# Kernel tuning notes

Hardware: AMD Instinct MI355X
Metric: run time of the kernel (lower is better)

Reference implementation:

```python
import jax, jax.numpy as jnp
import numpy as np

N_NODES = 50000


def _sage_conv(x, src, dst, W_l, b_l, W_r, n_nodes):
    # mean-aggregate neighbor (source) features onto targets
    msg = x[src]                                   # [E, d_in] gather
    agg = jax.ops.segment_sum(msg, dst, num_segments=n_nodes)   # [N, d_in]
    deg = jax.ops.segment_sum(jnp.ones((src.shape[0],), x.dtype), dst,
                              num_segments=n_nodes)
    agg = agg / jnp.clip(deg, 1.0, None)[:, None]  # mean with deg>=1 clamp (PyG)
    # out = lin_l(agg) + lin_r(x)   (bias lives in lin_l)
    return agg @ W_l.T + b_l + x @ W_r.T


def setup_inputs() -> dict:
    key = jax.random.key(0)
    ks = jax.random.split(key, 8)
    d_in, d_hid, d_out = 128, 256, 128
    n_edges = 800000
    x = jax.random.normal(ks[0], (N_NODES, d_in), dtype=jnp.float32)
    edge_index = jax.random.randint(ks[1], (2, n_edges), 0, N_NODES, dtype=jnp.int32)
    def glorot(k, shape):
        lim = float(np.sqrt(6.0 / (shape[0] + shape[1])))
        return jax.random.uniform(k, shape, jnp.float32, -lim, lim)
    return {
        "x": x,
        "edge_index": edge_index,
        "W1l": glorot(ks[2], (d_hid, d_in)),
        "b1": jnp.zeros((d_hid,), jnp.float32),
        "W1r": glorot(ks[3], (d_hid, d_in)),
        "W2l": glorot(ks[4], (d_out, d_hid)),
        "b2": jnp.zeros((d_out,), jnp.float32),
        "W2r": glorot(ks[5], (d_out, d_hid)),
    }


def reference(x, edge_index, W1l, b1, W1r, W2l, b2, W2r):
    src, dst = edge_index[0], edge_index[1]
    h = jax.nn.relu(_sage_conv(x, src, dst, W1l, b1, W1r, N_NODES))
    out = _sage_conv(h, src, dst, W2l, b2, W2r, N_NODES)
    return out
```

## Files before the change

kernel.cpp:

```cpp
#include <hip/hip_runtime.h>
#include <hip/hip_bf16.h>

#define NN 50000
#define NN_PAD 50176
#define NE 800000
#define NB 196
#define CAP 6144
#define EPB 4096

typedef __attribute__((ext_vector_type(8))) short short8;
typedef __attribute__((ext_vector_type(4))) float f32x4;
typedef __attribute__((ext_vector_type(2))) float f32x2;

__device__ __forceinline__ unsigned short f2bf(float f) {
    union { float f; unsigned u; } v; v.f = f;
    unsigned u = v.u;
    return (unsigned short)((u + 0x7fffu + ((u >> 16) & 1u)) >> 16);
}
__device__ __forceinline__ float bfu_lo(unsigned u) {
    union { unsigned u; float f; } v; v.u = u << 16; return v.f;
}
__device__ __forceinline__ float bfu_hi(unsigned u) {
    union { unsigned u; float f; } v; v.u = u & 0xffff0000u; return v.f;
}


__global__ void k_setup_part(const float* __restrict__ W1l, const float* __restrict__ W1r,
                             const float* __restrict__ W2l, const float* __restrict__ W2r,
                             unsigned short* __restrict__ W1pk, unsigned short* __restrict__ W2pk,
                             const float4* __restrict__ x4, unsigned short* __restrict__ Apk,
                             unsigned char* __restrict__ x_f8,
                             const int* __restrict__ src, const int* __restrict__ dst,
                             int* __restrict__ gcursor, unsigned* __restrict__ pairs) {
    int blk = blockIdx.x, t = threadIdx.x;
    if (blk < NB) {
        __shared__ int cnt[256];
        __shared__ int cur[256];
        __shared__ int base[256];
        cnt[t] = 0; cur[t] = 0;
        __syncthreads();
        int e0 = blk * EPB;
        int eend = min(e0 + EPB, NE);
        for (int e = e0 + t; e < eend; e += 256)
            atomicAdd(&cnt[dst[e] >> 8], 1);
        __syncthreads();
        if (t < NB && cnt[t] > 0) base[t] = t * CAP + atomicAdd(&gcursor[t], cnt[t]);
        __syncthreads();
        for (int e = e0 + t; e < eend; e += 256) {
            int s = src[e], d = dst[e];
            int bk = d >> 8;
            int pos = base[bk] + atomicAdd(&cur[bk], 1);
            if (pos < (bk + 1) * CAP) pairs[pos] = ((unsigned)s << 8) | (unsigned)(d & 255);
        }
    } else if (blk < 260) {
        int tid = (blk - 196) * 256 + t;
        int table = tid >> 13;
        int r = tid & 8191;
        int lane = r & 63, ni = (r >> 6) & 3, ks = (r >> 8) & 7, g = r >> 11;
        int lm = lane & 15, lq = lane >> 4;
        int o = g * 64 + ni * 16 + lm;
        int k = ks * 32 + lq * 8;
        unsigned short v[8];
        if (table == 0) {
            if (k < 128) {
#pragma unroll
                for (int j = 0; j < 8; ++j) v[j] = f2bf(W1l[o * 128 + k + j]);
            } else {
#pragma unroll
                for (int j = 0; j < 8; ++j) v[j] = f2bf(W1r[o * 128 + k - 128 + j]);
            }
            *(uint4*)(W1pk + (size_t)r * 8) = *(const uint4*)v;
        } else {
            if (o < 128) {
#pragma unroll
                for (int j = 0; j < 8; ++j) v[j] = f2bf(W2l[o * 256 + k + j]);
            } else {
#pragma unroll
                for (int j = 0; j < 8; ++j) v[j] = f2bf(W2r[(o - 128) * 256 + k + j]);
            }
            *(uint4*)(W2pk + (size_t)r * 8) = *(const uint4*)v;
        }
    } else {
        int gid = (blk - 260) * 256 + t;
        int n = gid >> 5, c = gid & 31;
        float4 v = x4[(size_t)n * 32 + c];
        unsigned short o[4];
        o[0] = f2bf(v.x); o[1] = f2bf(v.y); o[2] = f2bf(v.z); o[3] = f2bf(v.w);
        int k = 128 + c * 4;
        int ks = k >> 5, lq = (k >> 3) & 3, j0 = k & 7;
        int tile = n >> 6, r = n & 63, mi = r >> 4, lm = r & 15;
        *(uint2*)(Apk + (size_t)tile * 16384 +
                  ((size_t)((ks * 4 + mi) * 64 + lm + 16 * lq)) * 8 + j0) = *(const uint2*)o;
        unsigned p = (unsigned)__builtin_amdgcn_cvt_pk_fp8_f32(v.x, v.y, 0, false);
        p = (unsigned)__builtin_amdgcn_cvt_pk_fp8_f32(v.z, v.w, (int)p, true);
        *(unsigned*)(x_f8 + (size_t)n * 128 + c * 4) = p;
    }
}

__global__ void k_build(const int* __restrict__ gcursor, const unsigned* __restrict__ pairs,
                        unsigned* __restrict__ meta, unsigned short* __restrict__ esrc) {
    __shared__ int buf[256];
    __shared__ int ldeg[256];
    __shared__ int cur[256];
    __shared__ int sh_base, sh_cnt;
    __shared__ unsigned short lsrc[CAP];
    int b = blockIdx.x, t = threadIdx.x;
    int c = (t < NB) ? min(gcursor[t], CAP) : 0;
    buf[t] = c;
    __syncthreads();
#pragma unroll
    for (int o = 1; o < 256; o <<= 1) {
        int add = (t >= o) ? buf[t - o] : 0;
        __syncthreads();
        buf[t] += add;
        __syncthreads();
    }
    if (t == b) { sh_cnt = c; sh_base = buf[b] - c; }
    ldeg[t] = 0;
    __syncthreads();
    int cnt = sh_cnt, base = sh_base;
    for (int e = t; e < cnt; e += 256)
        atomicAdd(&ldeg[pairs[(size_t)b * CAP + e] & 255u], 1);
    __syncthreads();
    int v = ldeg[t];
    buf[t] = v;
    __syncthreads();
#pragma unroll
    for (int o = 1; o < 256; o <<= 1) {
        int add = (t >= o) ? buf[t - o] : 0;
        __syncthreads();
        buf[t] += add;
        __syncthreads();
    }
    int lst = buf[t] - v;
    cur[t] = lst;
    int node = b * 256 + t;
    meta[node] = (node < NN) ? ((unsigned)(base + lst) | ((unsigned)v << 20)) : 0u;
    __syncthreads();
    for (int e = t; e < cnt; e += 256) {
        unsigned p = pairs[(size_t)b * CAP + e];
        int pos = atomicAdd(&cur[p & 255u], 1);
        lsrc[pos] = (unsigned short)(p >> 8);
    }
    __syncthreads();
    for (int e = t; e < cnt; e += 256) esrc[base + e] = lsrc[e];
}

__global__ void k_agg1(const uint2* __restrict__ xf8, const unsigned* __restrict__ meta,
                       const unsigned short* __restrict__ esrc,
                       unsigned short* __restrict__ Apk) {
    int gid = blockIdx.x * blockDim.x + threadIdx.x;
    int n = gid >> 4, c = gid & 15;
    unsigned mt = meta[n];
    int st = (int)(mt & 0xFFFFFu), dg = (int)(mt >> 20);
    float acc[8] = {0.f, 0.f, 0.f, 0.f, 0.f, 0.f, 0.f, 0.f};
    int i = 0;
    for (; i + 2 <= dg; i += 2) {
        int s0 = esrc[st + i], s1 = esrc[st + i + 1];
        uint2 q0 = xf8[(size_t)s0 * 16 + c];
        uint2 q1 = xf8[(size_t)s1 * 16 + c];
        f32x2 a0 = __builtin_amdgcn_cvt_pk_f32_fp8(q0.x, false);
        f32x2 a1 = __builtin_amdgcn_cvt_pk_f32_fp8(q0.x, true);
        f32x2 a2 = __builtin_amdgcn_cvt_pk_f32_fp8(q0.y, false);
        f32x2 a3 = __builtin_amdgcn_cvt_pk_f32_fp8(q0.y, true);
        f32x2 b0 = __builtin_amdgcn_cvt_pk_f32_fp8(q1.x, false);
        f32x2 b1 = __builtin_amdgcn_cvt_pk_f32_fp8(q1.x, true);
        f32x2 b2 = __builtin_amdgcn_cvt_pk_f32_fp8(q1.y, false);
        f32x2 b3 = __builtin_amdgcn_cvt_pk_f32_fp8(q1.y, true);
        acc[0] += a0.x + b0.x; acc[1] += a0.y + b0.y;
        acc[2] += a1.x + b1.x; acc[3] += a1.y + b1.y;
        acc[4] += a2.x + b2.x; acc[5] += a2.y + b2.y;
        acc[6] += a3.x + b3.x; acc[7] += a3.y + b3.y;
    }
    if (i < dg) {
        int s = esrc[st + i];
        uint2 q0 = xf8[(size_t)s * 16 + c];
        f32x2 a0 = __builtin_amdgcn_cvt_pk_f32_fp8(q0.x, false);
        f32x2 a1 = __builtin_amdgcn_cvt_pk_f32_fp8(q0.x, true);
        f32x2 a2 = __builtin_amdgcn_cvt_pk_f32_fp8(q0.y, false);
        f32x2 a3 = __builtin_amdgcn_cvt_pk_f32_fp8(q0.y, true);
        acc[0] += a0.x; acc[1] += a0.y;
        acc[2] += a1.x; acc[3] += a1.y;
        acc[4] += a2.x; acc[5] += a2.y;
        acc[6] += a3.x; acc[7] += a3.y;
    }
    float invd = 1.0f / (float)max(dg, 1);
    unsigned short o[8];
#pragma unroll
    for (int j = 0; j < 8; ++j) o[j] = f2bf(acc[j] * invd);
    int ks = c >> 2, lq = c & 3;
    int tile = n >> 6, r = n & 63, mi = r >> 4, lm = r & 15;
    *(uint4*)(Apk + (size_t)tile * 16384 +
              ((size_t)((ks * 4 + mi) * 64 + lm + 16 * lq)) * 8) = *(const uint4*)o;
}

__global__ __launch_bounds__(256, 2) void k_gemm12(
        const unsigned short* __restrict__ Apk,
        const unsigned short* __restrict__ W1pk, const unsigned short* __restrict__ W2pk,
        const float* __restrict__ b1, const float* __restrict__ b2,
        unsigned char* __restrict__ y2f8, unsigned short* __restrict__ Sbf) {
    __shared__ unsigned short T[16384];
    int t = threadIdx.x, blk = blockIdx.x;
    int wave = t >> 6, lane = t & 63;
    int lm = lane & 15, lq = lane >> 4;
    int pbase = lm * 4 + lq;

    short8 w[8][4];
    {
        const unsigned short* wb = W1pk + (size_t)wave * 16384;
#pragma unroll
        for (int ks = 0; ks < 8; ++ks)
#pragma unroll
            for (int ni = 0; ni < 4; ++ni)
                w[ks][ni] = *(const short8*)(wb + ((size_t)((ks * 4 + ni) * 64 + lane)) * 8);
    }

    const unsigned short* apk = Apk + (size_t)blk * 16384;
    f32x4 acc1[4][4];
#pragma unroll
    for (int mi = 0; mi < 4; ++mi)
#pragma unroll
        for (int ni = 0; ni < 4; ++ni) acc1[mi][ni] = (f32x4){0.f, 0.f, 0.f, 0.f};
#pragma unroll
    for (int ks = 0; ks < 8; ++ks) {
        short8 a[4];
#pragma unroll
        for (int mi = 0; mi < 4; ++mi)
            a[mi] = *(const short8*)(apk + ((size_t)((ks * 4 + mi) * 64 + lane)) * 8);
#pragma unroll
        for (int mi = 0; mi < 4; ++mi)
#pragma unroll
            for (int ni = 0; ni < 4; ++ni)
                acc1[mi][ni] = __builtin_amdgcn_mfma_f32_16x16x32_bf16(a[mi], w[ks][ni], acc1[mi][ni], 0, 0, 0);
    }

    {
        const unsigned short* wb = W2pk + (size_t)wave * 16384;
#pragma unroll
        for (int ks = 0; ks < 8; ++ks)
#pragma unroll
            for (int ni = 0; ni < 4; ++ni)
                w[ks][ni] = *(const short8*)(wb + ((size_t)((ks * 4 + ni) * 64 + lane)) * 8);
    }

#pragma unroll
    for (int ni = 0; ni < 4; ++ni) {
        int col = wave * 64 + ni * 16 + lm;
        float bv = b1[col];
        int ks = col >> 5;
        int la = (col & 31) >> 3, j = col & 7;
#pragma unroll
        for (int mi = 0; mi < 4; ++mi)
#pragma unroll
            for (int r = 0; r < 4; ++r) {
                float v = fmaxf(acc1[mi][ni][r] + bv, 0.0f);
                T[((size_t)((ks * 4 + mi) * 64 + (lq * 4 + r) * 4 + la)) * 8 + j] = f2bf(v);
            }
    }
    __syncthreads();

    f32x4 acc2[4][4];
#pragma unroll
    for (int mi = 0; mi < 4; ++mi)
#pragma unroll
        for (int ni = 0; ni < 4; ++ni) acc2[mi][ni] = (f32x4){0.f, 0.f, 0.f, 0.f};
#pragma unroll
    for (int ks = 0; ks < 8; ++ks) {
        short8 a[4];
#pragma unroll
        for (int mi = 0; mi < 4; ++mi)
            a[mi] = *(const short8*)(T + ((size_t)((ks * 4 + mi) * 64 + pbase)) * 8);
#pragma unroll
        for (int mi = 0; mi < 4; ++mi)
#pragma unroll
            for (int ni = 0; ni < 4; ++ni)
                acc2[mi][ni] = __builtin_amdgcn_mfma_f32_16x16x32_bf16(a[mi], w[ks][ni], acc2[mi][ni], 0, 0, 0);
    }
    __syncthreads();

    {
        unsigned char* T8 = (unsigned char*)T;
        unsigned short* T16 = (unsigned short*)T + 4096;
        if (wave < 2) {
#pragma unroll
            for (int ni = 0; ni < 4; ++ni) {
                int col = wave * 64 + ni * 16 + lm;
#pragma unroll
                for (int mi = 0; mi < 4; ++mi)
#pragma unroll
                    for (int r = 0; r < 4; ++r) {
                        int rl = mi * 16 + lq * 4 + r;
                        float v = acc2[mi][ni][r];
                        unsigned p = (unsigned)__builtin_amdgcn_cvt_pk_fp8_f32(v, v, 0, false);
                        T8[rl * 128 + col] = (unsigned char)(p & 0xff);
                    }
            }
        } else {
#pragma unroll
            for (int ni = 0; ni < 4; ++ni) {
                int col = (wave - 2) * 64 + ni * 16 + lm;
                float bv = b2[col];
#pragma unroll
                for (int mi = 0; mi < 4; ++mi)
#pragma unroll
                    for (int r = 0; r < 4; ++r) {
                        int rl = mi * 16 + lq * 4 + r;
                        T16[rl * 128 + col] = f2bf(acc2[mi][ni][r] + bv);
                    }
            }
        }
    }
    __syncthreads();

    {
        const uint4* Ty = (const uint4*)T;
        uint4* gy = (uint4*)(y2f8 + (size_t)blk * 64 * 128);
        gy[t] = Ty[t];
        gy[t + 256] = Ty[t + 256];
        const uint4* Ts = (const uint4*)((const char*)T + 8192);
        uint4* gs = (uint4*)(Sbf + (size_t)blk * 64 * 128);
#pragma unroll
        for (int i = 0; i < 4; ++i) gs[t + i * 256] = Ts[t + i * 256];
    }
}

__global__ void k_agg_out(const uint2* __restrict__ yf8, const uint4* __restrict__ Sbf4,
                          const unsigned* __restrict__ meta,
                          const unsigned short* __restrict__ esrc,
                          float* __restrict__ out) {
    int gid = blockIdx.x * blockDim.x + threadIdx.x;
    int n = gid >> 4, c = gid & 15;
    unsigned mt = meta[n];
    int st = (int)(mt & 0xFFFFFu), dg = (int)(mt >> 20);
    float acc[8] = {0.f, 0.f, 0.f, 0.f, 0.f, 0.f, 0.f, 0.f};
    int i = 0;
    for (; i + 2 <= dg; i += 2) {
        int s0 = esrc[st + i], s1 = esrc[st + i + 1];
        uint2 q0 = yf8[(size_t)s0 * 16 + c];
        uint2 q1 = yf8[(size_t)s1 * 16 + c];
        f32x2 a0 = __builtin_amdgcn_cvt_pk_f32_fp8(q0.x, false);
        f32x2 a1 = __builtin_amdgcn_cvt_pk_f32_fp8(q0.x, true);
        f32x2 a2 = __builtin_amdgcn_cvt_pk_f32_fp8(q0.y, false);
        f32x2 a3 = __builtin_amdgcn_cvt_pk_f32_fp8(q0.y, true);
        f32x2 b0 = __builtin_amdgcn_cvt_pk_f32_fp8(q1.x, false);
        f32x2 b1 = __builtin_amdgcn_cvt_pk_f32_fp8(q1.x, true);
        f32x2 b2 = __builtin_amdgcn_cvt_pk_f32_fp8(q1.y, false);
        f32x2 b3 = __builtin_amdgcn_cvt_pk_f32_fp8(q1.y, true);
        acc[0] += a0.x + b0.x; acc[1] += a0.y + b0.y;
        acc[2] += a1.x + b1.x; acc[3] += a1.y + b1.y;
        acc[4] += a2.x + b2.x; acc[5] += a2.y + b2.y;
        acc[6] += a3.x + b3.x; acc[7] += a3.y + b3.y;
    }
    if (i < dg) {
        int s = esrc[st + i];
        uint2 q0 = yf8[(size_t)s * 16 + c];
        f32x2 a0 = __builtin_amdgcn_cvt_pk_f32_fp8(q0.x, false);
        f32x2 a1 = __builtin_amdgcn_cvt_pk_f32_fp8(q0.x, true);
        f32x2 a2 = __builtin_amdgcn_cvt_pk_f32_fp8(q0.y, false);
        f32x2 a3 = __builtin_amdgcn_cvt_pk_f32_fp8(q0.y, true);
        acc[0] += a0.x; acc[1] += a0.y;
        acc[2] += a1.x; acc[3] += a1.y;
        acc[4] += a2.x; acc[5] += a2.y;
        acc[6] += a3.x; acc[7] += a3.y;
    }
    float invd = 1.0f / (float)max(dg, 1);
    uint4 sv = Sbf4[(size_t)n * 16 + c];
    float4 o0, o1;
    o0.x = bfu_lo(sv.x) + acc[0] * invd; o0.y = bfu_hi(sv.x) + acc[1] * invd;
    o0.z = bfu_lo(sv.y) + acc[2] * invd; o0.w = bfu_hi(sv.y) + acc[3] * invd;
    o1.x = bfu_lo(sv.z) + acc[4] * invd; o1.y = bfu_hi(sv.z) + acc[5] * invd;
    o1.z = bfu_lo(sv.w) + acc[6] * invd; o1.w = bfu_hi(sv.w) + acc[7] * invd;
    float* op = out + (size_t)n * 128 + c * 8;
    *(float4*)op = o0; *(float4*)(op + 4) = o1;
}

extern "C" void kernel_launch(void* const* d_in, const int* in_sizes, int n_in,
                              void* d_out, int out_size, void* d_ws, size_t ws_size,
                              hipStream_t stream) {
    const float* x   = (const float*)d_in[0];
    const int*   ei  = (const int*)d_in[1];
    const int*   src = ei;
    const int*   dst = ei + NE;
    const float* W1l = (const float*)d_in[2];
    const float* b1  = (const float*)d_in[3];
    const float* W1r = (const float*)d_in[4];
    const float* W2l = (const float*)d_in[5];
    const float* b2  = (const float*)d_in[6];
    const float* W2r = (const float*)d_in[7];
    float* out = (float*)d_out;

    char* ws = (char*)d_ws;
    unsigned* meta        = (unsigned*)(ws + 0);
    int* gcursor          = (int*)(ws + 401408);
    unsigned short* esrc  = (unsigned short*)(ws + 409600);
    unsigned* pairs       = (unsigned*)(ws + 4194304);
    unsigned short* Sbf   = (unsigned short*)(ws + 9437184);
    unsigned char* x_f8   = (unsigned char*)(ws + 22282240);
    unsigned char* y2f8   = (unsigned char*)(ws + 28704768);
    unsigned short* Apk   = (unsigned short*)(ws + 35651584);
    unsigned short* W1pk  = (unsigned short*)(ws + 61341696);
    unsigned short* W2pk  = (unsigned short*)(ws + 61472768);

    hipMemsetAsync(gcursor, 0, 1024, stream);
    k_setup_part<<<6510, 256, 0, stream>>>(W1l, W1r, W2l, W2r, W1pk, W2pk,
                                           (const float4*)x, Apk, x_f8, src, dst,
                                           gcursor, pairs);
    k_build<<<NB, 256, 0, stream>>>(gcursor, pairs, meta, esrc);
    k_agg1<<<NN * 16 / 256, 256, 0, stream>>>((const uint2*)x_f8, meta, esrc, Apk);
    k_gemm12<<<NN_PAD / 64, 256, 0, stream>>>(Apk, W1pk, W2pk, b1, b2, y2f8, Sbf);
    k_agg_out<<<NN * 16 / 256, 256, 0, stream>>>((const uint2*)y2f8, (const uint4*)Sbf,
                                                 meta, esrc, out);
}
```

Before: 186.1 us.

## Fuse layer-1 neighbor aggregation into GEMM kernel via shared-memory staging

Removes the separate k_agg1 kernel. The GEMM kernel now gathers and averages the fp8 neighbor features for its own 64-row tile, writes them into shared memory, and also copies the row-major bf16 x into the packed A layout in shared memory. This saves one launch and the global round trip of the packed A buffer. Other changes: k_build caches the pairs array in LDS instead of reading it twice, the gather loops are unrolled by four, and non-temporal loads and stores are used for streaming buffers. The risks are lower overlap inside the GEMM kernel, since gather latency now sits before the MFMA work at only 2 blocks per CU, and the added 24KB of LDS in k_build.

```diff
diff --git a/kernel.cpp b/kernel.cpp
--- a/kernel.cpp
+++ b/kernel.cpp
@@ -11,6 +11,8 @@
 typedef __attribute__((ext_vector_type(8))) short short8;
 typedef __attribute__((ext_vector_type(4))) float f32x4;
 typedef __attribute__((ext_vector_type(2))) float f32x2;
+typedef __attribute__((ext_vector_type(4))) unsigned int u32x4;
+typedef __attribute__((ext_vector_type(2))) unsigned int u32x2;
 
 __device__ __forceinline__ unsigned short f2bf(float f) {
     union { float f; unsigned u; } v; v.f = f;
@@ -23,12 +25,20 @@
 __device__ __forceinline__ float bfu_hi(unsigned u) {
     union { unsigned u; float f; } v; v.u = u & 0xffff0000u; return v.f;
 }
+__device__ __forceinline__ void acc_fp8(float* acc, uint2 q) {
+    f32x2 a0 = __builtin_amdgcn_cvt_pk_f32_fp8(q.x, false);
+    f32x2 a1 = __builtin_amdgcn_cvt_pk_f32_fp8(q.x, true);
+    f32x2 a2 = __builtin_amdgcn_cvt_pk_f32_fp8(q.y, false);
+    f32x2 a3 = __builtin_amdgcn_cvt_pk_f32_fp8(q.y, true);
+    acc[0] += a0.x; acc[1] += a0.y; acc[2] += a1.x; acc[3] += a1.y;
+    acc[4] += a2.x; acc[5] += a2.y; acc[6] += a3.x; acc[7] += a3.y;
+}
 
 
 __global__ void k_setup_part(const float* __restrict__ W1l, const float* __restrict__ W1r,
                              const float* __restrict__ W2l, const float* __restrict__ W2r,
                              unsigned short* __restrict__ W1pk, unsigned short* __restrict__ W2pk,
-                             const float4* __restrict__ x4, unsigned short* __restrict__ Apk,
+                             const float* __restrict__ x, unsigned short* __restrict__ xbf,
                              unsigned char* __restrict__ x_f8,
                              const int* __restrict__ src, const int* __restrict__ dst,
                              int* __restrict__ gcursor, unsigned* __restrict__ pairs) {
@@ -83,16 +93,12 @@
     } else {
         int gid = (blk - 260) * 256 + t;
         int n = gid >> 5, c = gid & 31;
-        float4 v = x4[(size_t)n * 32 + c];
+        f32x4 v = __builtin_nontemporal_load((const f32x4*)x + (size_t)n * 32 + c);
         unsigned short o[4];
-        o[0] = f2bf(v.x); o[1] = f2bf(v.y); o[2] = f2bf(v.z); o[3] = f2bf(v.w);
-        int k = 128 + c * 4;
-        int ks = k >> 5, lq = (k >> 3) & 3, j0 = k & 7;
-        int tile = n >> 6, r = n & 63, mi = r >> 4, lm = r & 15;
-        *(uint2*)(Apk + (size_t)tile * 16384 +
-                  ((size_t)((ks * 4 + mi) * 64 + lm + 16 * lq)) * 8 + j0) = *(const uint2*)o;
-        unsigned p = (unsigned)__builtin_amdgcn_cvt_pk_fp8_f32(v.x, v.y, 0, false);
-        p = (unsigned)__builtin_amdgcn_cvt_pk_fp8_f32(v.z, v.w, (int)p, true);
+        o[0] = f2bf(v[0]); o[1] = f2bf(v[1]); o[2] = f2bf(v[2]); o[3] = f2bf(v[3]);
+        *(u32x2*)(xbf + (size_t)n * 128 + c * 4) = *(const u32x2*)o;
+        unsigned p = (unsigned)__builtin_amdgcn_cvt_pk_fp8_f32(v[0], v[1], 0, false);
+        p = (unsigned)__builtin_amdgcn_cvt_pk_fp8_f32(v[2], v[3], (int)p, true);
         *(unsigned*)(x_f8 + (size_t)n * 128 + c * 4) = p;
     }
 }
@@ -104,6 +110,7 @@
     __shared__ int cur[256];
     __shared__ int sh_base, sh_cnt;
     __shared__ unsigned short lsrc[CAP];
+    __shared__ unsigned lp[CAP];
     int b = blockIdx.x, t = threadIdx.x;
     int c = (t < NB) ? min(gcursor[t], CAP) : 0;
     buf[t] = c;
@@ -119,8 +126,11 @@
     ldeg[t] = 0;
     __syncthreads();
     int cnt = sh_cnt, base = sh_base;
-    for (int e = t; e < cnt; e += 256)
-        atomicAdd(&ldeg[pairs[(size_t)b * CAP + e] & 255u], 1);
+    for (int e = t; e < cnt; e += 256) {
+        unsigned p = pairs[(size_t)b * CAP + e];
+        lp[e] = p;
+        atomicAdd(&ldeg[p & 255u], 1);
+    }
     __syncthreads();
     int v = ldeg[t];
     buf[t] = v;
@@ -138,7 +148,7 @@
     meta[node] = (node < NN) ? ((unsigned)(base + lst) | ((unsigned)v << 20)) : 0u;
     __syncthreads();
     for (int e = t; e < cnt; e += 256) {
-        unsigned p = pairs[(size_t)b * CAP + e];
+        unsigned p = lp[e];
         int pos = atomicAdd(&cur[p & 255u], 1);
         lsrc[pos] = (unsigned short)(p >> 8);
     }
@@ -146,56 +156,9 @@
     for (int e = t; e < cnt; e += 256) esrc[base + e] = lsrc[e];
 }
 
-__global__ void k_agg1(const uint2* __restrict__ xf8, const unsigned* __restrict__ meta,
-                       const unsigned short* __restrict__ esrc,
-                       unsigned short* __restrict__ Apk) {
-    int gid = blockIdx.x * blockDim.x + threadIdx.x;
-    int n = gid >> 4, c = gid & 15;
-    unsigned mt = meta[n];
-    int st = (int)(mt & 0xFFFFFu), dg = (int)(mt >> 20);
-    float acc[8] = {0.f, 0.f, 0.f, 0.f, 0.f, 0.f, 0.f, 0.f};
-    int i = 0;
-    for (; i + 2 <= dg; i += 2) {
-        int s0 = esrc[st + i], s1 = esrc[st + i + 1];
-        uint2 q0 = xf8[(size_t)s0 * 16 + c];
-        uint2 q1 = xf8[(size_t)s1 * 16 + c];
-        f32x2 a0 = __builtin_amdgcn_cvt_pk_f32_fp8(q0.x, false);
-        f32x2 a1 = __builtin_amdgcn_cvt_pk_f32_fp8(q0.x, true);
-        f32x2 a2 = __builtin_amdgcn_cvt_pk_f32_fp8(q0.y, false);
-        f32x2 a3 = __builtin_amdgcn_cvt_pk_f32_fp8(q0.y, true);
-        f32x2 b0 = __builtin_amdgcn_cvt_pk_f32_fp8(q1.x, false);
-        f32x2 b1 = __builtin_amdgcn_cvt_pk_f32_fp8(q1.x, true);
-        f32x2 b2 = __builtin_amdgcn_cvt_pk_f32_fp8(q1.y, false);
-        f32x2 b3 = __builtin_amdgcn_cvt_pk_f32_fp8(q1.y, true);
-        acc[0] += a0.x + b0.x; acc[1] += a0.y + b0.y;
-        acc[2] += a1.x + b1.x; acc[3] += a1.y + b1.y;
-        acc[4] += a2.x + b2.x; acc[5] += a2.y + b2.y;
-        acc[6] += a3.x + b3.x; acc[7] += a3.y + b3.y;
-    }
-    if (i < dg) {
-        int s = esrc[st + i];
-        uint2 q0 = xf8[(size_t)s * 16 + c];
-        f32x2 a0 = __builtin_amdgcn_cvt_pk_f32_fp8(q0.x, false);
-        f32x2 a1 = __builtin_amdgcn_cvt_pk_f32_fp8(q0.x, true);
-        f32x2 a2 = __builtin_amdgcn_cvt_pk_f32_fp8(q0.y, false);
-        f32x2 a3 = __builtin_amdgcn_cvt_pk_f32_fp8(q0.y, true);
-        acc[0] += a0.x; acc[1] += a0.y;
-        acc[2] += a1.x; acc[3] += a1.y;
-        acc[4] += a2.x; acc[5] += a2.y;
-        acc[6] += a3.x; acc[7] += a3.y;
-    }
-    float invd = 1.0f / (float)max(dg, 1);
-    unsigned short o[8];
-#pragma unroll
-    for (int j = 0; j < 8; ++j) o[j] = f2bf(acc[j] * invd);
-    int ks = c >> 2, lq = c & 3;
-    int tile = n >> 6, r = n & 63, mi = r >> 4, lm = r & 15;
-    *(uint4*)(Apk + (size_t)tile * 16384 +
-              ((size_t)((ks * 4 + mi) * 64 + lm + 16 * lq)) * 8) = *(const uint4*)o;
-}
-
 __global__ __launch_bounds__(256, 2) void k_gemm12(
-        const unsigned short* __restrict__ Apk,
+        const unsigned short* __restrict__ xbf, const uint2* __restrict__ xf8,
+        const unsigned* __restrict__ meta, const unsigned short* __restrict__ esrc,
         const unsigned short* __restrict__ W1pk, const unsigned short* __restrict__ W2pk,
         const float* __restrict__ b1, const float* __restrict__ b2,
         unsigned char* __restrict__ y2f8, unsigned short* __restrict__ Sbf) {
@@ -215,7 +178,49 @@
                 w[ks][ni] = *(const short8*)(wb + ((size_t)((ks * 4 + ni) * 64 + lane)) * 8);
     }
 
-    const unsigned short* apk = Apk + (size_t)blk * 16384;
+    {
+        int cc = t & 15, rb = t >> 4;
+        int ks2 = cc >> 2, lq2 = cc & 3;
+        for (int mi2 = 0; mi2 < 4; ++mi2) {
+            int n = blk * 64 + mi2 * 16 + rb;
+            unsigned mt = meta[n];
+            int st = (int)(mt & 0xFFFFFu), dg = (int)(mt >> 20);
+            float acc[8] = {0.f, 0.f, 0.f, 0.f, 0.f, 0.f, 0.f, 0.f};
+            int i = 0;
+            for (; i + 4 <= dg; i += 4) {
+                int s0 = esrc[st + i],     s1 = esrc[st + i + 1];
+                int s2 = esrc[st + i + 2], s3 = esrc[st + i + 3];
+                uint2 q0 = xf8[(size_t)s0 * 16 + cc];
+                uint2 q1 = xf8[(size_t)s1 * 16 + cc];
+                uint2 q2 = xf8[(size_t)s2 * 16 + cc];
+                uint2 q3 = xf8[(size_t)s3 * 16 + cc];
+                acc_fp8(acc, q0); acc_fp8(acc, q1); acc_fp8(acc, q2); acc_fp8(acc, q3);
+            }
+            for (; i < dg; ++i) {
+                int s = esrc[st + i];
+                acc_fp8(acc, xf8[(size_t)s * 16 + cc]);
+            }
+            float invd = 1.0f / (float)max(dg, 1);
+            unsigned short o[8];
+#pragma unroll
+            for (int j = 0; j < 8; ++j) o[j] = f2bf(acc[j] * invd);
+            *(u32x4*)(T + ((size_t)((ks2 * 4 + mi2) * 64 + rb + 16 * lq2)) * 8) = *(const u32x4*)o;
+        }
+    }
+    {
+        int r = t >> 2, d0 = (t & 3) * 32;
+        int mi2 = r >> 4, lmr = r & 15;
+        const unsigned short* xr = xbf + (size_t)(blk * 64 + r) * 128 + d0;
+#pragma unroll
+        for (int q = 0; q < 4; ++q) {
+            u32x4 v = __builtin_nontemporal_load((const u32x4*)xr + q);
+            int d = d0 + q * 8;
+            int ks2 = 4 + (d >> 5), lq2 = (d >> 3) & 3;
+            *(u32x4*)(T + ((size_t)((ks2 * 4 + mi2) * 64 + lmr + 16 * lq2)) * 8) = v;
+        }
+    }
+    __syncthreads();
+
     f32x4 acc1[4][4];
 #pragma unroll
     for (int mi = 0; mi < 4; ++mi)
@@ -226,7 +231,7 @@
         short8 a[4];
 #pragma unroll
         for (int mi = 0; mi < 4; ++mi)
-            a[mi] = *(const short8*)(apk + ((size_t)((ks * 4 + mi) * 64 + lane)) * 8);
+            a[mi] = *(const short8*)(T + ((size_t)((ks * 4 + mi) * 64 + lane)) * 8);
 #pragma unroll
         for (int mi = 0; mi < 4; ++mi)
 #pragma unroll
@@ -242,6 +247,7 @@
             for (int ni = 0; ni < 4; ++ni)
                 w[ks][ni] = *(const short8*)(wb + ((size_t)((ks * 4 + ni) * 64 + lane)) * 8);
     }
+    __syncthreads();
 
 #pragma unroll
     for (int ni = 0; ni < 4; ++ni) {
@@ -317,14 +323,15 @@
         uint4* gy = (uint4*)(y2f8 + (size_t)blk * 64 * 128);
         gy[t] = Ty[t];
         gy[t + 256] = Ty[t + 256];
-        const uint4* Ts = (const uint4*)((const char*)T + 8192);
-        uint4* gs = (uint4*)(Sbf + (size_t)blk * 64 * 128);
-#pragma unroll
-        for (int i = 0; i < 4; ++i) gs[t + i * 256] = Ts[t + i * 256];
-    }
-}
-
-__global__ void k_agg_out(const uint2* __restrict__ yf8, const uint4* __restrict__ Sbf4,
+        const u32x4* Ts = (const u32x4*)((const char*)T + 8192);
+        u32x4* gs = (u32x4*)(Sbf + (size_t)blk * 64 * 128);
+#pragma unroll
+        for (int i = 0; i < 4; ++i)
+            __builtin_nontemporal_store(Ts[t + i * 256], &gs[t + i * 256]);
+    }
+}
+
+__global__ void k_agg_out(const uint2* __restrict__ yf8, const unsigned short* __restrict__ Sbf,
                           const unsigned* __restrict__ meta,
                           const unsigned short* __restrict__ esrc,
                           float* __restrict__ out) {
@@ -334,44 +341,29 @@
     int st = (int)(mt & 0xFFFFFu), dg = (int)(mt >> 20);
     float acc[8] = {0.f, 0.f, 0.f, 0.f, 0.f, 0.f, 0.f, 0.f};
     int i = 0;
-    for (; i + 2 <= dg; i += 2) {
-        int s0 = esrc[st + i], s1 = esrc[st + i + 1];
+    for (; i + 4 <= dg; i += 4) {
+        int s0 = esrc[st + i],     s1 = esrc[st + i + 1];
+        int s2 = esrc[st + i + 2], s3 = esrc[st + i + 3];
         uint2 q0 = yf8[(size_t)s0 * 16 + c];
         uint2 q1 = yf8[(size_t)s1 * 16 + c];
-        f32x2 a0 = __builtin_amdgcn_cvt_pk_f32_fp8(q0.x, false);
-        f32x2 a1 = __builtin_amdgcn_cvt_pk_f32_fp8(q0.x, true);
-        f32x2 a2 = __builtin_amdgcn_cvt_pk_f32_fp8(q0.y, false);
-        f32x2 a3 = __builtin_amdgcn_cvt_pk_f32_fp8(q0.y, true);
-        f32x2 b0 = __builtin_amdgcn_cvt_pk_f32_fp8(q1.x, false);
-        f32x2 b1 = __builtin_amdgcn_cvt_pk_f32_fp8(q1.x, true);
-        f32x2 b2 = __builtin_amdgcn_cvt_pk_f32_fp8(q1.y, false);
-        f32x2 b3 = __builtin_amdgcn_cvt_pk_f32_fp8(q1.y, true);
-        acc[0] += a0.x + b0.x; acc[1] += a0.y + b0.y;
-        acc[2] += a1.x + b1.x; acc[3] += a1.y + b1.y;
-        acc[4] += a2.x + b2.x; acc[5] += a2.y + b2.y;
-        acc[6] += a3.x + b3.x; acc[7] += a3.y + b3.y;
-    }
-    if (i < dg) {
+        uint2 q2 = yf8[(size_t)s2 * 16 + c];
+        uint2 q3 = yf8[(size_t)s3 * 16 + c];
+        acc_fp8(acc, q0); acc_fp8(acc, q1); acc_fp8(acc, q2); acc_fp8(acc, q3);
+    }
+    for (; i < dg; ++i) {
         int s = esrc[st + i];
-        uint2 q0 = yf8[(size_t)s * 16 + c];
-        f32x2 a0 = __builtin_amdgcn_cvt_pk_f32_fp8(q0.x, false);
-        f32x2 a1 = __builtin_amdgcn_cvt_pk_f32_fp8(q0.x, true);
-        f32x2 a2 = __builtin_amdgcn_cvt_pk_f32_fp8(q0.y, false);
-        f32x2 a3 = __builtin_amdgcn_cvt_pk_f32_fp8(q0.y, true);
-        acc[0] += a0.x; acc[1] += a0.y;
-        acc[2] += a1.x; acc[3] += a1.y;
-        acc[4] += a2.x; acc[5] += a2.y;
-        acc[6] += a3.x; acc[7] += a3.y;
+        acc_fp8(acc, yf8[(size_t)s * 16 + c]);
     }
     float invd = 1.0f / (float)max(dg, 1);
-    uint4 sv = Sbf4[(size_t)n * 16 + c];
-    float4 o0, o1;
-    o0.x = bfu_lo(sv.x) + acc[0] * invd; o0.y = bfu_hi(sv.x) + acc[1] * invd;
-    o0.z = bfu_lo(sv.y) + acc[2] * invd; o0.w = bfu_hi(sv.y) + acc[3] * invd;
-    o1.x = bfu_lo(sv.z) + acc[4] * invd; o1.y = bfu_hi(sv.z) + acc[5] * invd;
-    o1.z = bfu_lo(sv.w) + acc[6] * invd; o1.w = bfu_hi(sv.w) + acc[7] * invd;
-    float* op = out + (size_t)n * 128 + c * 8;
-    *(float4*)op = o0; *(float4*)(op + 4) = o1;
+    u32x4 sv = __builtin_nontemporal_load((const u32x4*)Sbf + (size_t)n * 16 + c);
+    f32x4 o0, o1;
+    o0[0] = bfu_lo(sv[0]) + acc[0] * invd; o0[1] = bfu_hi(sv[0]) + acc[1] * invd;
+    o0[2] = bfu_lo(sv[1]) + acc[2] * invd; o0[3] = bfu_hi(sv[1]) + acc[3] * invd;
+    o1[0] = bfu_lo(sv[2]) + acc[4] * invd; o1[1] = bfu_hi(sv[2]) + acc[5] * invd;
+    o1[2] = bfu_lo(sv[3]) + acc[6] * invd; o1[3] = bfu_hi(sv[3]) + acc[7] * invd;
+    f32x4* op = (f32x4*)(out + (size_t)n * 128 + c * 8);
+    __builtin_nontemporal_store(o0, op);
+    __builtin_nontemporal_store(o1, op + 1);
 }
 
 extern "C" void kernel_launch(void* const* d_in, const int* in_sizes, int n_in,
@@ -391,23 +383,22 @@
 
     char* ws = (char*)d_ws;
     unsigned* meta        = (unsigned*)(ws + 0);
-    int* gcursor          = (int*)(ws + 401408);
-    unsigned short* esrc  = (unsigned short*)(ws + 409600);
-    unsigned* pairs       = (unsigned*)(ws + 4194304);
-    unsigned short* Sbf   = (unsigned short*)(ws + 9437184);
-    unsigned char* x_f8   = (unsigned char*)(ws + 22282240);
-    unsigned char* y2f8   = (unsigned char*)(ws + 28704768);
-    unsigned short* Apk   = (unsigned short*)(ws + 35651584);
-    unsigned short* W1pk  = (unsigned short*)(ws + 61341696);
-    unsigned short* W2pk  = (unsigned short*)(ws + 61472768);
+    int* gcursor          = (int*)(ws + 204800);
+    unsigned short* esrc  = (unsigned short*)(ws + 208896);
+    unsigned* pairs       = (unsigned*)(ws + 2097152);
+    unsigned short* Sbf   = (unsigned short*)(ws + 8388608);
+    unsigned char* x_f8   = (unsigned char*)(ws + 25165824);
+    unsigned char* y2f8   = (unsigned char*)(ws + 33554432);
+    unsigned short* xbf   = (unsigned short*)(ws + 41943040);
+    unsigned short* W1pk  = (unsigned short*)(ws + 56623104);
+    unsigned short* W2pk  = (unsigned short*)(ws + 56754176);
 
     hipMemsetAsync(gcursor, 0, 1024, stream);
     k_setup_part<<<6510, 256, 0, stream>>>(W1l, W1r, W2l, W2r, W1pk, W2pk,
-                                           (const float4*)x, Apk, x_f8, src, dst,
-                                           gcursor, pairs);
+                                           x, xbf, x_f8, src, dst, gcursor, pairs);
     k_build<<<NB, 256, 0, stream>>>(gcursor, pairs, meta, esrc);
-    k_agg1<<<NN * 16 / 256, 256, 0, stream>>>((const uint2*)x_f8, meta, esrc, Apk);
-    k_gemm12<<<NN_PAD / 64, 256, 0, stream>>>(Apk, W1pk, W2pk, b1, b2, y2f8, Sbf);
-    k_agg_out<<<NN * 16 / 256, 256, 0, stream>>>((const uint2*)y2f8, (const uint4*)Sbf,
+    k_gemm12<<<NN_PAD / 64, 256, 0, stream>>>(xbf, (const uint2*)x_f8, meta, esrc,
+                                              W1pk, W2pk, b1, b2, y2f8, Sbf);
+    k_agg_out<<<NN * 16 / 256, 256, 0, stream>>>((const uint2*)y2f8, Sbf,
                                                  meta, esrc, out);
 }
```

New measurement: 204.2 us. 9.7% more time.
